# Kernel optimization log

Hardware: AMD Instinct MI355X
Metric: run time of the kernel (lower is better)

## Reference

```python
import jax, jax.numpy as jnp
import numpy as np

B, S, D = 16, 4096, 64
N_HASHES = 8
BUCKET_SIZE = 64
N_BUCKETS = S // BUCKET_SIZE  # 64
NEG = -5e4  # the module uses -50000.0 as masking value
EPS = 1e-6


def setup_inputs() -> dict:
    key = jax.random.key(0)
    k1, k2, k3 = jax.random.split(key, 3)
    qk = jax.random.normal(k1, (B, S, D), dtype=jnp.float32)
    v = jax.random.normal(k2, (B, S, D), dtype=jnp.float32)
    # random rotations for LSH: (batch, dim, n_hashes, n_buckets//2)
    rotations = jax.random.normal(k3, (B, D, N_HASHES, N_BUCKETS // 2), dtype=jnp.float32)
    return {"qk": qk, "v": v, "rotations": rotations, "seed_": 0}


def _look_one_back(x):
    # prepend previous chunk (with wraparound) along the key axis
    x_extra = jnp.concatenate([x[:, -1:], x[:, :-1]], axis=1)
    return jnp.concatenate([x, x_extra], axis=2)


def reference(qk, v, rotations, seed_):
    b, s, d = qk.shape
    n_hashes = rotations.shape[2]
    n_buckets = 2 * rotations.shape[3]
    chunks = n_hashes * n_buckets  # n_bins == n_buckets

    # ---- hash_vectors ----
    rot = jnp.einsum('btf,bfhi->bhti', qk, rotations)          # (b, h, s, nb/2)
    rot = jnp.concatenate([rot, -rot], axis=-1)                # (b, h, s, nb)
    buckets = jnp.argmax(rot, axis=-1)                         # (b, h, s)
    offsets = (jnp.arange(n_hashes) * n_buckets)[None, :, None]
    buckets = (buckets + offsets).reshape(b, n_hashes * s)     # (b, h*s)

    # ---- sort by (bucket, position) ----
    ticker = jnp.arange(n_hashes * s)
    buckets_and_t = s * buckets + (ticker % s)[None, :]
    sticker = jnp.argsort(buckets_and_t, axis=-1)              # stable sort indices
    undo_sort = jnp.argsort(sticker, axis=-1)

    st = sticker % s                                           # original positions
    sqk = jnp.take_along_axis(qk, st[..., None], axis=1)       # (b, h*s, d)
    sv = jnp.take_along_axis(v, st[..., None], axis=1)

    bq_t = st.reshape(b, chunks, -1)                           # (b, chunks, bucket)
    bqk = sqk.reshape(b, chunks, -1, d)
    bv = sv.reshape(b, chunks, -1, d)

    bq = bqk
    norm = jnp.linalg.norm(bqk, axis=-1, keepdims=True)
    bk = bqk / (norm + EPS)                                    # make_unit_length

    bk = _look_one_back(bk)                                    # (b, chunks, 2*bucket, d)
    bv = _look_one_back(bv)
    bkv_t = _look_one_back(bq_t[..., None])[..., 0]            # (b, chunks, 2*bucket)

    dots = jnp.einsum('bhie,bhje->bhij', bq, bk) * (d ** -0.5)
    self_mask = bq_t[:, :, :, None] == bkv_t[:, :, None, :]
    dots = jnp.where(self_mask, NEG, dots)

    dots_lse = jax.nn.logsumexp(dots, axis=-1, keepdims=True)  # (b, chunks, bucket, 1)
    probs = jnp.exp(dots - dots_lse)
    bo = jnp.einsum('buij,buje->buie', probs, bv)              # (b, chunks, bucket, d)

    so = bo.reshape(b, n_hashes * s, d)
    slogits = dots_lse.reshape(b, n_hashes * s)

    # ---- unsort ----
    o = jnp.take_along_axis(so, undo_sort[..., None], axis=1)
    logits = jnp.take_along_axis(slogits, undo_sort, axis=-1)

    # ---- combine hash rounds via logsumexp weights ----
    o = o.reshape(b, n_hashes, s, d)
    logits = logits.reshape(b, n_hashes, s, 1)
    w = jnp.exp(logits - jax.nn.logsumexp(logits, axis=1, keepdims=True))
    out = jnp.sum(o * w, axis=1)                               # (b, s, d)
    return out, buckets
```

## Files before the change

kernel.cpp:

```cpp
#include <hip/hip_runtime.h>
#include <math.h>

#define BB   16
#define SS   4096
#define DD   64
#define HH   8
#define NBH  32
#define NB   64
#define NCH  512

typedef __attribute__((ext_vector_type(8))) short s16x8;
typedef __attribute__((ext_vector_type(4))) short s16x4;
typedef __attribute__((ext_vector_type(4))) float f32x4;
typedef __attribute__((ext_vector_type(4))) unsigned u32x4;

static __device__ __forceinline__ unsigned short f2bf(float x) {
  union { float f; unsigned u; } a; a.f = x;
  unsigned r = a.u + 0x7fffu + ((a.u >> 16) & 1u);
  return (unsigned short)(r >> 16);
}
static __device__ __forceinline__ float bf2f(unsigned short u) {
  union { unsigned u; float f; } a; a.u = ((unsigned)u) << 16;
  return a.f;
}
static __device__ __forceinline__ unsigned bfrnd_hi(float x) {
  union { float f; unsigned u; } a; a.f = x;
  return a.u + 0x7fffu + ((a.u >> 16) & 1u);
}
static __device__ __forceinline__ unsigned pack_bf(float lo, float hi) {
  return __builtin_amdgcn_perm(bfrnd_hi(hi), bfrnd_hi(lo), 0x07060302u);
}

__global__ __launch_bounds__(256) void k_conv(
    const float* __restrict__ qk, const float* __restrict__ v,
    unsigned short* __restrict__ qb, unsigned short* __restrict__ kb,
    unsigned short* __restrict__ vb) {
  const int gid = blockIdx.x * 256 + threadIdx.x;
  const int half = BB * SS * 4;
  const bool isV = gid >= half;
  const int id = isV ? gid - half : gid;
  const int row = id >> 2, q4 = id & 3;

  const float4* src =
      (const float4*)((isV ? v : qk) + (size_t)row * DD + q4 * 16);
  float vals[16];
#pragma unroll
  for (int g = 0; g < 4; g++) {
    const float4 a = src[g];
    vals[g * 4 + 0] = a.x; vals[g * 4 + 1] = a.y;
    vals[g * 4 + 2] = a.z; vals[g * 4 + 3] = a.w;
  }

  if (!isV) {
    float ss = 0.f;
#pragma unroll
    for (int i = 0; i < 16; i++) ss += vals[i] * vals[i];
    ss += __shfl_xor(ss, 1);
    ss += __shfl_xor(ss, 2);
    const float scl = 0.125f / (sqrtf(ss) + 1e-6f);
    unsigned short qo[16], ko[16];
#pragma unroll
    for (int i = 0; i < 16; i++) {
      qo[i] = f2bf(vals[i]);
      ko[i] = f2bf(vals[i] * scl);
    }
    unsigned short* qd = qb + (size_t)row * DD + q4 * 16;
    unsigned short* kd = kb + (size_t)row * DD + q4 * 16;
    *(s16x8*)qd = *(const s16x8*)&qo[0];
    *(s16x8*)(qd + 8) = *(const s16x8*)&qo[8];
    *(s16x8*)kd = *(const s16x8*)&ko[0];
    *(s16x8*)(kd + 8) = *(const s16x8*)&ko[8];
  } else {
    unsigned short vo[16];
#pragma unroll
    for (int i = 0; i < 16; i++) vo[i] = f2bf(vals[i]);
    unsigned short* vd = vb + (size_t)row * DD + q4 * 16;
    *(s16x8*)vd = *(const s16x8*)&vo[0];
    *(s16x8*)(vd + 8) = *(const s16x8*)&vo[8];
  }
}

__global__ __launch_bounds__(256) void k_rotT(
    const float* __restrict__ rot, unsigned short* __restrict__ rTh,
    unsigned short* __restrict__ rTl, int* __restrict__ needy_count) {
  __shared__ float slab[32][256];
  const int b = blockIdx.x;
  const int tid = threadIdx.x;
  if (b == 0 && tid == 0) *needy_count = 0;

  for (int st = 0; st < 2; st++) {
#pragma unroll
    for (int fr = 0; fr < 32; fr++)
      slab[fr][tid] = rot[(size_t)b * (DD * HH * NBH) +
                          (size_t)(st * 32 + fr) * 256 + tid];
    __syncthreads();
    unsigned short hi[32], lo[32];
#pragma unroll
    for (int fr = 0; fr < 32; fr++) {
      const float x = slab[fr][tid];
      const unsigned short hh = f2bf(x);
      hi[fr] = hh;
      lo[fr] = f2bf(x - bf2f(hh));
    }
    unsigned short* dh = rTh + ((size_t)b * 256 + tid) * DD + st * 32;
    unsigned short* dl = rTl + ((size_t)b * 256 + tid) * DD + st * 32;
#pragma unroll
    for (int g = 0; g < 4; g++) {
      *(s16x8*)(dh + g * 8) = *(const s16x8*)&hi[g * 8];
      *(s16x8*)(dl + g * 8) = *(const s16x8*)&lo[g * 8];
    }
    __syncthreads();
  }
}

#define MARGIN 1e-2f

__global__ __launch_bounds__(256, 2) void k_hash_mfma(
    const float* __restrict__ qk, const unsigned short* __restrict__ rTh,
    const unsigned short* __restrict__ rTl, int* __restrict__ bucket_local,
    float* __restrict__ buckets_out, int* __restrict__ needy_list,
    int* __restrict__ needy_count) {
  __shared__ struct __align__(16) {
    unsigned short ah[128][72];
    unsigned short al[128][72];
    float sc[128][33];
  } sm;
  const int b = blockIdx.x;
  const int t0 = blockIdx.y * 128;
  const int tid = threadIdx.x;
  const int w = tid >> 6, lane = tid & 63;
  const int quad = lane >> 4, l16 = lane & 15;

  {
    const int row = tid >> 1, hf = tid & 1;
    const float4* src =
        (const float4*)(qk + ((size_t)b * SS + t0 + row) * DD + hf * 32);
#pragma unroll
    for (int gg = 0; gg < 4; gg++) {
      const float4 v0 = src[gg * 2], v1 = src[gg * 2 + 1];
      const float a[8] = {v0.x, v0.y, v0.z, v0.w, v1.x, v1.y, v1.z, v1.w};
      unsigned short hi[8], lo[8];
#pragma unroll
      for (int e = 0; e < 8; e++) {
        const unsigned short hh = f2bf(a[e]);
        hi[e] = hh;
        lo[e] = f2bf(a[e] - bf2f(hh));
      }
      *(s16x8*)&sm.ah[row][hf * 32 + gg * 8] = *(const s16x8*)hi;
      *(s16x8*)&sm.al[row][hf * 32 + gg * 8] = *(const s16x8*)lo;
    }
  }
  __syncthreads();

  s16x8 Ah[2][2], Al[2][2];
#pragma unroll
  for (int mtl = 0; mtl < 2; mtl++) {
    const int row = (w * 2 + mtl) * 16 + l16;
#pragma unroll
    for (int ks = 0; ks < 2; ks++) {
      Ah[mtl][ks] = *(const s16x8*)&sm.ah[row][ks * 32 + quad * 8];
      Al[mtl][ks] = *(const s16x8*)&sm.al[row][ks * 32 + quad * 8];
    }
  }

#pragma unroll 1
  for (int h = 0; h < HH; h++) {
#pragma unroll
    for (int nt = 0; nt < 2; nt++) {
      const size_t rrow = (((size_t)b * HH + h) * 32 + nt * 16 + l16) * DD;
      s16x8 Bh2[2], Bl2[2];
#pragma unroll
      for (int ks = 0; ks < 2; ks++) {
        Bh2[ks] = *(const s16x8*)&rTh[rrow + ks * 32 + quad * 8];
        Bl2[ks] = *(const s16x8*)&rTl[rrow + ks * 32 + quad * 8];
      }
#pragma unroll
      for (int mtl = 0; mtl < 2; mtl++) {
        f32x4 acc = (f32x4){0.f, 0.f, 0.f, 0.f};
#pragma unroll
        for (int ks = 0; ks < 2; ks++) {
          acc = __builtin_amdgcn_mfma_f32_16x16x32_bf16(Al[mtl][ks], Bl2[ks], acc, 0, 0, 0);
          acc = __builtin_amdgcn_mfma_f32_16x16x32_bf16(Al[mtl][ks], Bh2[ks], acc, 0, 0, 0);
          acc = __builtin_amdgcn_mfma_f32_16x16x32_bf16(Ah[mtl][ks], Bl2[ks], acc, 0, 0, 0);
          acc = __builtin_amdgcn_mfma_f32_16x16x32_bf16(Ah[mtl][ks], Bh2[ks], acc, 0, 0, 0);
        }
#pragma unroll
        for (int r = 0; r < 4; r++)
          sm.sc[(w * 2 + mtl) * 16 + quad * 4 + r][nt * 16 + l16] = acc[r];
      }
    }
    __syncthreads();

    {
      const int l32 = lane & 31;
      const int tloc = w * 32 + l32;
      const bool neg = lane >= 32;
      const float sgn = neg ? -1.0f : 1.0f;
      float best = -3.0e38f, second = -3.0e38f;
      int bi = 0;
#pragma unroll 8
      for (int i = 0; i < 32; i++) {
        const float vv = sgn * sm.sc[tloc][i];
        if (vv > best) { second = best; best = vv; bi = i; }
        else if (vv > second) second = vv;
      }
      if (neg) bi += 32;
      const float ob = __shfl_xor(best, 32);
      const float os = __shfl_xor(second, 32);
      const int obi = __shfl_xor(bi, 32);
      if (lane < 32) {
        const float ms = fmaxf(fminf(best, ob), fmaxf(second, os));
        float mb = best; int mbi = bi;
        if (ob > best) { mb = ob; mbi = obi; }
        const int t = t0 + tloc;
        bucket_local[((size_t)b * HH + h) * SS + t] = mbi;
        buckets_out[(size_t)b * (HH * SS) + (size_t)h * SS + t] =
            (float)(h * NB + mbi);
        if (mb - ms <= MARGIN) {
          const int slot = atomicAdd(needy_count, 1);
          needy_list[slot] = (((b << 3) | h) << 12) | t;
        }
      }
    }
    __syncthreads();
  }
}

__global__ __launch_bounds__(256) void k_hash_fix(
    const float* __restrict__ qk, const float* __restrict__ rot,
    const int* __restrict__ needy_list, const int* __restrict__ needy_count,
    int* __restrict__ bucket_local, float* __restrict__ buckets_out) {
  const int n = *needy_count;
  const int hw = (blockIdx.x * 256 + (int)threadIdx.x) >> 5;
  const int li = threadIdx.x & 31;
  const int nhw = gridDim.x * 8;

  for (int idx = hw; idx < n; idx += nhw) {
    const int code = needy_list[idx];
    const int t = code & 4095;
    const int bh = code >> 12;
    const int b = bh >> 3, h = bh & 7;

    const float* qrow = qk + ((size_t)b * SS + t) * DD;
    const float* rcol = rot + ((size_t)b * DD * HH + h) * NBH + li;

    double acc = 0.0;
#pragma unroll 8
    for (int f = 0; f < DD; f++)
      acc += (double)qrow[f] * (double)rcol[(size_t)f * (HH * NBH)];

    double bv = acc;
    int bi = li;
    if (-acc > bv) { bv = -acc; bi = li + 32; }
#pragma unroll
    for (int off = 1; off < 32; off <<= 1) {
      const double ov = __shfl_xor(bv, off);
      const int oi = __shfl_xor(bi, off);
      if (ov > bv || (ov == bv && oi < bi)) { bv = ov; bi = oi; }
    }
    if (li == 0) {
      bucket_local[((size_t)b * HH + h) * SS + t] = bi;
      buckets_out[(size_t)b * (HH * SS) + (size_t)h * SS + t] =
          (float)(h * NB + bi);
    }
  }
}

__global__ __launch_bounds__(256) void k_sort(
    const int* __restrict__ bucket_local, int* __restrict__ sort_t,
    int* __restrict__ ipos) {
  __shared__ unsigned short lb[SS];
  __shared__ unsigned char  cnt[NB][256];
  __shared__ unsigned short pfx[NB][256];
  __shared__ int part[NB][4];
  __shared__ int tot[NB];
  __shared__ int base[NB];

  const int bh = blockIdx.x;
  const int tid = threadIdx.x;
  const int* src = bucket_local + (size_t)bh * SS;

  int* czero = (int*)&cnt[0][0];
#pragma unroll
  for (int i = 0; i < 16; i++) czero[tid + i * 256] = 0;
  __syncthreads();

#pragma unroll
  for (int i = 0; i < 16; i++) {
    const int t = tid * 16 + i;
    const int v = src[t];
    lb[t] = (unsigned short)v;
    cnt[v][tid]++;
  }
  __syncthreads();

  {
    const int bk = tid & 63, sg = tid >> 6;
    int s = 0;
#pragma unroll 8
    for (int i = 0; i < 64; i++) s += cnt[bk][sg * 64 + i];
    part[bk][sg] = s;
  }
  __syncthreads();
  if (tid < NB) tot[tid] = part[tid][0] + part[tid][1] + part[tid][2] + part[tid][3];
  __syncthreads();
  if (tid == 0) {
    int r = 0;
    for (int i = 0; i < NB; i++) { base[i] = r; r += tot[i]; }
  }
  __syncthreads();
  {
    const int bk = tid & 63, sg = tid >> 6;
    int run = base[bk];
    for (int s = 0; s < sg; s++) run += part[bk][s];
#pragma unroll 8
    for (int i = 0; i < 64; i++) {
      const int th = sg * 64 + i;
      pfx[bk][th] = (unsigned short)run;
      run += cnt[bk][th];
    }
  }
  __syncthreads();
  int* st = sort_t + (size_t)bh * SS;
  int* ip = ipos + (size_t)bh * SS;
#pragma unroll
  for (int i = 0; i < 16; i++) {
    const int t = tid * 16 + i;
    const int bk = lb[t];
    const int pos = pfx[bk][tid]++;
    st[pos] = t;
    ip[t] = pos;
  }
}

__global__ __launch_bounds__(256, 4) void k_attn2(
    const unsigned short* __restrict__ qb, const unsigned short* __restrict__ kbg,
    const unsigned short* __restrict__ vbg, const int* __restrict__ sort_t,
    unsigned short* __restrict__ so, float* __restrict__ lse_u) {
  const int blk = blockIdx.x;
  const int b = blk >> 9;
  const int c = blk & 511;
  const int h = c >> 6, cc = c & 63;
  const int cp = (c + 511) & 511;
  const int hp = cp >> 6, ccp = cp & 63;

  __shared__ struct __align__(16) {
    union {
      unsigned short kb[128][72];
      unsigned short p[64][136];
      float olds[64][68];
    } kp;
    unsigned short vsT[64][136];
    int tk[128];
  } sm;

  const int tid = threadIdx.x;
  const int w = tid >> 6;
  const int lane = tid & 63;
  const int quad = lane >> 4;
  const int l16 = lane & 15;

  if (tid < 128) {
    const size_t srci = (tid < 64)
        ? (((size_t)b * HH + h) * SS + cc * 64 + tid)
        : (((size_t)b * HH + hp) * SS + ccp * 64 + (tid - 64));
    sm.tk[tid] = sort_t[srci];
  }
  __syncthreads();

  {
    const int j = tid >> 1, hf = tid & 1;
    const int trow = sm.tk[j];
    const s16x8* ksrc = (const s16x8*)(kbg + ((size_t)b * SS + trow) * DD + hf * 32);
    s16x8 kr[4];
#pragma unroll
    for (int g = 0; g < 4; g++) kr[g] = ksrc[g];
#pragma unroll
    for (int g = 0; g < 4; g++)
      *(s16x8*)&sm.kp.kb[j][hf * 32 + g * 8] = kr[g];
  }
  {
    const int fg = tid >> 5;
    const int tg = (tid & 31) << 2;
    const unsigned short* vb_b = vbg + (size_t)b * SS * DD + fg * 8;
    const u32x4 a0v = *(const u32x4*)(vb_b + (size_t)sm.tk[tg + 0] * DD);
    const u32x4 a1v = *(const u32x4*)(vb_b + (size_t)sm.tk[tg + 1] * DD);
    const u32x4 a2v = *(const u32x4*)(vb_b + (size_t)sm.tk[tg + 2] * DD);
    const u32x4 a3v = *(const u32x4*)(vb_b + (size_t)sm.tk[tg + 3] * DD);
#pragma unroll
    for (int j = 0; j < 4; j++) {
      uint2 ev, ov;
      ev.x = __builtin_amdgcn_perm(a1v[j], a0v[j], 0x05040100u);
      ev.y = __builtin_amdgcn_perm(a3v[j], a2v[j], 0x05040100u);
      ov.x = __builtin_amdgcn_perm(a1v[j], a0v[j], 0x07060302u);
      ov.y = __builtin_amdgcn_perm(a3v[j], a2v[j], 0x07060302u);
      *(uint2*)&sm.vsT[fg * 8 + 2 * j][tg] = ev;
      *(uint2*)&sm.vsT[fg * 8 + 2 * j + 1][tg] = ov;
    }
  }
  const int tq = sm.tk[w * 16 + l16];
  const unsigned short* qrowp = qb + ((size_t)b * SS + tq) * DD;
  const s16x8 a0 = *(const s16x8*)(qrowp + quad * 8);
  const s16x8 a1 = *(const s16x8*)(qrowp + 32 + quad * 8);
  __syncthreads();

  f32x4 acc[8];
#pragma unroll
  for (int nt = 0; nt < 8; nt++) acc[nt] = (f32x4){0.f, 0.f, 0.f, 0.f};
#pragma unroll
  for (int nt = 0; nt < 8; nt++) {
    const s16x8 b0 = *(const s16x8*)&sm.kp.kb[nt * 16 + l16][quad * 8];
    const s16x8 b1 = *(const s16x8*)&sm.kp.kb[nt * 16 + l16][32 + quad * 8];
    acc[nt] = __builtin_amdgcn_mfma_f32_16x16x32_bf16(b0, a0, acc[nt], 0, 0, 0);
    acc[nt] = __builtin_amdgcn_mfma_f32_16x16x32_bf16(b1, a1, acc[nt], 0, 0, 0);
  }

  {
    const bool dm = (quad == (l16 >> 2));
    const int rm = l16 & 3;
#pragma unroll
    for (int nt = 0; nt < 4; nt++)
      if (nt == w) {
#pragma unroll
        for (int r = 0; r < 4; r++)
          if (dm && rm == r) acc[nt][r] = -50000.0f;
      }
  }
  if (cc == 0) {
#pragma unroll
    for (int nt = 4; nt < 8; nt++)
#pragma unroll
      for (int r = 0; r < 4; r++)
        if (sm.tk[nt * 16 + quad * 4 + r] == tq) acc[nt][r] = -50000.0f;
  }

  float mv[8];
#pragma unroll
  for (int nt = 0; nt < 8; nt++)
    mv[nt] = fmaxf(fmaxf(acc[nt][0], acc[nt][1]), fmaxf(acc[nt][2], acc[nt][3]));
  float m = fmaxf(fmaxf(fmaxf(mv[0], mv[1]), fmaxf(mv[2], mv[3])),
                  fmaxf(fmaxf(mv[4], mv[5]), fmaxf(mv[6], mv[7])));
  m = fmaxf(m, __shfl_xor(m, 16));
  m = fmaxf(m, __shfl_xor(m, 32));

  float sv[8];
#pragma unroll
  for (int nt = 0; nt < 8; nt++) {
#pragma unroll
    for (int r = 0; r < 4; r++) acc[nt][r] = __expf(acc[nt][r] - m);
    sv[nt] = (acc[nt][0] + acc[nt][1]) + (acc[nt][2] + acc[nt][3]);
  }
  float s = ((sv[0] + sv[1]) + (sv[2] + sv[3])) +
            ((sv[4] + sv[5]) + (sv[6] + sv[7]));
  s += __shfl_xor(s, 16);
  s += __shfl_xor(s, 32);
  const float inv = 1.0f / s;
  const float lse = __logf(s) + m;

  if (quad == 0)
    lse_u[((size_t)b * SS + tq) * HH + h] = lse;

  __syncthreads();

  {
    const int prow = w * 16 + l16;
#pragma unroll
    for (int nt = 0; nt < 8; nt++) {
      uint2 pv;
      pv.x = pack_bf(acc[nt][0] * inv, acc[nt][1] * inv);
      pv.y = pack_bf(acc[nt][2] * inv, acc[nt][3] * inv);
      *(uint2*)&sm.kp.p[prow][nt * 16 + quad * 4] = pv;
    }
  }
  __syncthreads();

  f32x4 o[4];
#pragma unroll
  for (int nt = 0; nt < 4; nt++) o[nt] = (f32x4){0.f, 0.f, 0.f, 0.f};
  const unsigned short* vrow = &sm.vsT[w * 16 + l16][0];
#pragma unroll
  for (int kc = 0; kc < 4; kc++) {
    const s16x8 av = *(const s16x8*)(vrow + kc * 32 + quad * 8);
#pragma unroll
    for (int nt = 0; nt < 4; nt++) {
      const s16x8 bp = *(const s16x8*)&sm.kp.p[nt * 16 + l16][kc * 32 + quad * 8];
      o[nt] = __builtin_amdgcn_mfma_f32_16x16x32_bf16(av, bp, o[nt], 0, 0, 0);
    }
  }

  __syncthreads();

#pragma unroll
  for (int nt = 0; nt < 4; nt++)
    *(f32x4*)&sm.kp.olds[nt * 16 + l16][w * 16 + quad * 4] = o[nt];
  __syncthreads();

  {
    const int q = tid >> 2, qt = tid & 3;
    const int t = sm.tk[q];
    float vals[16];
    *(f32x4*)&vals[0]  = *(const f32x4*)&sm.kp.olds[q][qt * 16 + 0];
    *(f32x4*)&vals[4]  = *(const f32x4*)&sm.kp.olds[q][qt * 16 + 4];
    *(f32x4*)&vals[8]  = *(const f32x4*)&sm.kp.olds[q][qt * 16 + 8];
    *(f32x4*)&vals[12] = *(const f32x4*)&sm.kp.olds[q][qt * 16 + 12];
    unsigned pk[8];
#pragma unroll
    for (int g = 0; g < 8; g++) pk[g] = pack_bf(vals[2 * g], vals[2 * g + 1]);
    unsigned short* dst =
        so + (((size_t)b * SS + t) * HH + h) * DD + qt * 16;
    *(uint4*)dst = *(const uint4*)&pk[0];
    *(uint4*)(dst + 8) = *(const uint4*)&pk[4];
  }
}

__global__ __launch_bounds__(256) void k_combine2(
    const unsigned short* __restrict__ so, const float* __restrict__ lse_u,
    float* __restrict__ out) {
  const size_t idx = (size_t)blockIdx.x * 256 + threadIdx.x;
  const int f = (int)(idx & 63);
  const size_t bt = idx >> 6;

  float l[HH];
#pragma unroll
  for (int h = 0; h < HH; h++) l[h] = lse_u[bt * HH + h];
  float m = l[0];
#pragma unroll
  for (int h = 1; h < HH; h++) m = fmaxf(m, l[h]);
  float den = 0.f, num = 0.f;
#pragma unroll
  for (int h = 0; h < HH; h++) {
    const float wgt = __expf(l[h] - m);
    den += wgt;
    num += wgt * bf2f(so[(bt * HH + h) * DD + f]);
  }
  out[idx] = num / den;
}

__global__ __launch_bounds__(256, 2) void k_hash_f32(
    const float* __restrict__ qk, const float* __restrict__ rot,
    int* __restrict__ bucket_local, float* __restrict__ buckets_out,
    int* __restrict__ needy_list, int* __restrict__ needy_count) {
  __shared__ float lb[128 * 65];
  const int b = blockIdx.x;
  const int t0 = blockIdx.y * 128;
  const int tid = threadIdx.x;

  {
    const int row = tid >> 1, hf = (tid & 1) * 32;
    const float4* src =
        (const float4*)(qk + ((size_t)b * SS + t0 + row) * DD + hf);
    float* dst = &lb[row * 65 + hf];
#pragma unroll
    for (int g = 0; g < 8; g++) {
      const float4 vv = src[g];
      dst[g * 4 + 0] = vv.x; dst[g * 4 + 1] = vv.y;
      dst[g * 4 + 2] = vv.z; dst[g * 4 + 3] = vv.w;
    }
  }
  __syncthreads();

  const int w = tid >> 6;
  const int l = tid & 63;
  const int hb = __builtin_amdgcn_readfirstlane(w);

  for (int hp = 0; hp < 2; hp++) {
    const int h = hb + hp * 4;
    const float* rbase = rot + ((size_t)b * DD * HH + h) * NBH;
    const size_t rstride = HH * NBH;

    float acc0[NBH], acc1[NBH];
#pragma unroll
    for (int i = 0; i < NBH; i++) { acc0[i] = 0.f; acc1[i] = 0.f; }

    float4 bufA[8], bufB[8];
#pragma unroll
    for (int i4 = 0; i4 < 8; i4++) bufA[i4] = ((const float4*)rbase)[i4];

    for (int f = 0; f < DD; f += 2) {
      {
        const float4* r4 = (const float4*)(rbase + (size_t)(f + 1) * rstride);
#pragma unroll
        for (int i4 = 0; i4 < 8; i4++) bufB[i4] = r4[i4];
      }
      {
        const float q0 = lb[l * 65 + f];
        const float q1 = lb[(l + 64) * 65 + f];
#pragma unroll
        for (int i4 = 0; i4 < 8; i4++) {
          const float4 rv = bufA[i4];
          acc0[i4*4+0] = fmaf(q0, rv.x, acc0[i4*4+0]);
          acc0[i4*4+1] = fmaf(q0, rv.y, acc0[i4*4+1]);
          acc0[i4*4+2] = fmaf(q0, rv.z, acc0[i4*4+2]);
          acc0[i4*4+3] = fmaf(q0, rv.w, acc0[i4*4+3]);
          acc1[i4*4+0] = fmaf(q1, rv.x, acc1[i4*4+0]);
          acc1[i4*4+1] = fmaf(q1, rv.y, acc1[i4*4+1]);
          acc1[i4*4+2] = fmaf(q1, rv.z, acc1[i4*4+2]);
          acc1[i4*4+3] = fmaf(q1, rv.w, acc1[i4*4+3]);
        }
      }
      if (f + 2 < DD) {
        const float4* r4 = (const float4*)(rbase + (size_t)(f + 2) * rstride);
#pragma unroll
        for (int i4 = 0; i4 < 8; i4++) bufA[i4] = r4[i4];
      }
      {
        const float q0 = lb[l * 65 + f + 1];
        const float q1 = lb[(l + 64) * 65 + f + 1];
#pragma unroll
        for (int i4 = 0; i4 < 8; i4++) {
          const float4 rv = bufB[i4];
          acc0[i4*4+0] = fmaf(q0, rv.x, acc0[i4*4+0]);
          acc0[i4*4+1] = fmaf(q0, rv.y, acc0[i4*4+1]);
          acc0[i4*4+2] = fmaf(q0, rv.z, acc0[i4*4+2]);
          acc0[i4*4+3] = fmaf(q0, rv.w, acc0[i4*4+3]);
          acc1[i4*4+0] = fmaf(q1, rv.x, acc1[i4*4+0]);
          acc1[i4*4+1] = fmaf(q1, rv.y, acc1[i4*4+1]);
          acc1[i4*4+2] = fmaf(q1, rv.z, acc1[i4*4+2]);
          acc1[i4*4+3] = fmaf(q1, rv.w, acc1[i4*4+3]);
        }
      }
    }

#pragma unroll
    for (int tok = 0; tok < 2; tok++) {
      const float* acc = tok ? acc1 : acc0;
      float best = -3.0e38f, second = -3.0e38f;
      int bi = 0;
#pragma unroll
      for (int i = 0; i < 64; i++) {
        const float vv = (i < NBH) ? acc[i] : -acc[i - NBH];
        if (vv > best) { second = best; best = vv; bi = i; }
        else if (vv > second) { second = vv; }
      }
      const int t = t0 + tok * 64 + l;
      bucket_local[((size_t)b * HH + h) * SS + t] = bi;
      buckets_out[(size_t)b * (HH * SS) + (size_t)h * SS + t] =
          (float)(h * NB + bi);
      if (best - second <= MARGIN) {
        const int slot = atomicAdd(needy_count, 1);
        needy_list[slot] = (((b << 3) | h) << 12) | t;
      }
    }
  }
}

__global__ __launch_bounds__(256) void k_attn_atomic(
    const float* __restrict__ qk, const float* __restrict__ v,
    const int* __restrict__ sort_t, float* __restrict__ num,
    float* __restrict__ den) {
  const int blk = blockIdx.x;
  const int b = blk >> 9;
  const int c = blk & 511;
  const int h = c >> 6, cc = c & 63;
  const int cp = (c + 511) & 511;
  const int hp = cp >> 6, ccp = cp & 63;

  __shared__ union {
    struct {
      float qt[DD * 64];
      float kt[DD * 128];
      int   tq[64];
      int   tk[128];
      float nrm[128];
      float red[16 * 64];
      float rmax[64];
      float rsum[64];
    } a;
    struct {
      float pt[128 * 64];
      float vs[128 * 64];
    } p;
  } sm;

  const int tid = threadIdx.x;

  if (tid < 64)
    sm.a.tq[tid] = sort_t[((size_t)b * HH + h) * SS + cc * 64 + tid];
  if (tid >= 128) {
    const int j = tid - 128;
    const size_t src = (j < 64) ? (((size_t)b * HH + h) * SS + cc * 64 + j)
                                : (((size_t)b * HH + hp) * SS + ccp * 64 + (j - 64));
    sm.a.tk[j] = sort_t[src];
  }
  if (tid >= 64 && tid < 192) sm.a.nrm[tid - 64] = 0.f;
  __syncthreads();

  {
    const int qi = tid >> 2, qq = tid & 3;
    const float4* qsrc =
        (const float4*)(qk + ((size_t)b * SS + sm.a.tq[qi]) * DD) + qq * 4;
#pragma unroll
    for (int k4 = 0; k4 < 4; k4++) {
      float4 val = qsrc[k4];
      const int f = qq * 16 + k4 * 4;
      sm.a.qt[(f + 0) * 64 + qi] = val.x;
      sm.a.qt[(f + 1) * 64 + qi] = val.y;
      sm.a.qt[(f + 2) * 64 + qi] = val.z;
      sm.a.qt[(f + 3) * 64 + qi] = val.w;
    }
    const int j = tid >> 1, hhf = tid & 1;
    const float4* ksrc =
        (const float4*)(qk + ((size_t)b * SS + sm.a.tk[j]) * DD) + hhf * 8;
    float ss = 0.f;
#pragma unroll
    for (int k4 = 0; k4 < 8; k4++) {
      float4 val = ksrc[k4];
      const int f = hhf * 32 + k4 * 4;
      sm.a.kt[(f + 0) * 128 + j] = val.x;
      sm.a.kt[(f + 1) * 128 + j] = val.y;
      sm.a.kt[(f + 2) * 128 + j] = val.z;
      sm.a.kt[(f + 3) * 128 + j] = val.w;
      ss += val.x * val.x + val.y * val.y + val.z * val.z + val.w * val.w;
    }
    atomicAdd(&sm.a.nrm[j], ss);
  }
  __syncthreads();
  if (tid < 128) {
    const float n = sqrtf(sm.a.nrm[tid]) + 1e-6f;
    sm.a.nrm[tid] = 0.125f / n;
  }
  float4 vreg[8];
  {
    const int j = tid >> 1, hhf = tid & 1;
    const float4* vsrc =
        (const float4*)(v + ((size_t)b * SS + sm.a.tk[j]) * DD) + hhf * 8;
#pragma unroll
    for (int k4 = 0; k4 < 8; k4++) vreg[k4] = vsrc[k4];
  }
  __syncthreads();

  const int qi0 = (tid & 15) * 4;
  const int j0g = (tid >> 4) * 8;
  const int kg = tid >> 4;
  float acc[4][8];
#pragma unroll
  for (int i = 0; i < 4; i++)
#pragma unroll
    for (int j = 0; j < 8; j++) acc[i][j] = 0.f;

#pragma unroll 8
  for (int f = 0; f < DD; f++) {
    float4 qv = *(const float4*)&sm.a.qt[f * 64 + qi0];
    float4 k0 = *(const float4*)&sm.a.kt[f * 128 + j0g];
    float4 k1 = *(const float4*)&sm.a.kt[f * 128 + j0g + 4];
    float qa[4] = {qv.x, qv.y, qv.z, qv.w};
    float ka[8] = {k0.x, k0.y, k0.z, k0.w, k1.x, k1.y, k1.z, k1.w};
#pragma unroll
    for (int i = 0; i < 4; i++)
#pragma unroll
      for (int j = 0; j < 8; j++) acc[i][j] = fmaf(qa[i], ka[j], acc[i][j]);
  }

  int tqr[4];
#pragma unroll
  for (int i = 0; i < 4; i++) tqr[i] = sm.a.tq[qi0 + i];
  int tkr[8]; float scl[8];
#pragma unroll
  for (int j = 0; j < 8; j++) {
    tkr[j] = sm.a.tk[j0g + j];
    scl[j] = sm.a.nrm[j0g + j];
  }
#pragma unroll
  for (int i = 0; i < 4; i++)
#pragma unroll
    for (int j = 0; j < 8; j++) {
      const float dv = acc[i][j] * scl[j];
      acc[i][j] = (tqr[i] == tkr[j]) ? -50000.0f : dv;
    }

  float pmax[4];
#pragma unroll
  for (int i = 0; i < 4; i++) {
    float m = acc[i][0];
#pragma unroll
    for (int j = 1; j < 8; j++) m = fmaxf(m, acc[i][j]);
    pmax[i] = m;
  }
#pragma unroll
  for (int i = 0; i < 4; i++) sm.a.red[kg * 64 + qi0 + i] = pmax[i];
  __syncthreads();
  if (tid < 64) {
    float m = -3.0e38f;
#pragma unroll
    for (int g = 0; g < 16; g++) m = fmaxf(m, sm.a.red[g * 64 + tid]);
    sm.a.rmax[tid] = m;
  }
  __syncthreads();
  float psum[4];
#pragma unroll
  for (int i = 0; i < 4; i++) {
    const float rm = sm.a.rmax[qi0 + i];
    float s = 0.f;
#pragma unroll
    for (int j = 0; j < 8; j++) {
      const float e = __expf(acc[i][j] - rm);
      acc[i][j] = e;
      s += e;
    }
    psum[i] = s;
  }
#pragma unroll
  for (int i = 0; i < 4; i++) sm.a.red[kg * 64 + qi0 + i] = psum[i];
  __syncthreads();
  if (tid < 64) {
    float s = 0.f;
#pragma unroll
    for (int g = 0; g < 16; g++) s += sm.a.red[g * 64 + tid];
    sm.a.rsum[tid] = s;
  }
  __syncthreads();
  float lse[4], isum[4];
#pragma unroll
  for (int i = 0; i < 4; i++) {
    const float rm = sm.a.rmax[qi0 + i];
    const float s = sm.a.rsum[qi0 + i];
    isum[i] = 1.0f / s;
    lse[i] = __logf(s) + rm;
  }
  __syncthreads();

#pragma unroll
  for (int j = 0; j < 8; j++)
#pragma unroll
    for (int i = 0; i < 4; i++)
      sm.p.pt[(j0g + j) * 64 + qi0 + i] = acc[i][j] * isum[i];
  {
    const int j = tid >> 1, hhf = tid & 1;
#pragma unroll
    for (int k4 = 0; k4 < 8; k4++)
      *(float4*)&sm.p.vs[j * 64 + hhf * 32 + k4 * 4] = vreg[k4];
  }
  __syncthreads();

  const int f0 = (tid >> 4) * 4;
  float o[4][4];
#pragma unroll
  for (int i = 0; i < 4; i++)
#pragma unroll
    for (int j = 0; j < 4; j++) o[i][j] = 0.f;

#pragma unroll 8
  for (int j = 0; j < 128; j++) {
    float4 pv = *(const float4*)&sm.p.pt[j * 64 + qi0];
    float4 vv = *(const float4*)&sm.p.vs[j * 64 + f0];
    float pa[4] = {pv.x, pv.y, pv.z, pv.w};
    float va[4] = {vv.x, vv.y, vv.z, vv.w};
#pragma unroll
    for (int i = 0; i < 4; i++)
#pragma unroll
      for (int j2 = 0; j2 < 4; j2++) o[i][j2] = fmaf(pa[i], va[j2], o[i][j2]);
  }

#pragma unroll
  for (int i = 0; i < 4; i++) {
    const float w = __expf(lse[i]);
    float* dst = num + ((size_t)b * SS + tqr[i]) * DD + f0;
#pragma unroll
    for (int j = 0; j < 4; j++) atomicAdd(dst + j, o[i][j] * w);
    if (kg == 0) atomicAdd(den + (size_t)b * SS + tqr[i], w);
  }
}

__global__ __launch_bounds__(256) void k_final(float* __restrict__ o,
                                               const float* __restrict__ den) {
  const size_t i = (size_t)blockIdx.x * 256 + threadIdx.x;
  o[i] = o[i] / den[i >> 6];
}

extern "C" void kernel_launch(void* const* d_in, const int* in_sizes, int n_in,
                              void* d_out, int out_size, void* d_ws,
                              size_t ws_size, hipStream_t stream) {
  const float* qk  = (const float*)d_in[0];
  const float* v   = (const float*)d_in[1];
  const float* rot = (const float*)d_in[2];

  float* out_attn = (float*)d_out;
  float* buckets_out = out_attn + (size_t)BB * SS * DD;

  const size_t BHS = (size_t)BB * HH * SS;
  const size_t BSD = (size_t)BB * SS * DD;
  const size_t RT  = (size_t)BB * HH * 32 * DD;
  int* bucket_local = (int*)d_ws;
  int* sort_t = bucket_local + BHS;
  int* ipos = sort_t + BHS;
  float* lse_u = (float*)(ipos + BHS);
  unsigned short* qb16 = (unsigned short*)(lse_u + BHS);
  unsigned short* kb16 = qb16 + BSD;
  unsigned short* vb16 = kb16 + BSD;
  unsigned short* so_u = vb16 + BSD;
  unsigned short* rTh = so_u + BHS * DD;
  unsigned short* rTl = rTh + RT;

  const size_t NEED2 =
      4 * BHS * 4 + 3 * BSD * 2 + BHS * DD * 2 + 2 * RT * 2;

  if (ws_size >= NEED2) {
    k_conv<<<2 * BB * SS * 4 / 256, 256, 0, stream>>>(qk, v, qb16, kb16, vb16);
    k_rotT<<<BB, 256, 0, stream>>>(rot, rTh, rTl, ipos);
    k_hash_mfma<<<dim3(BB, SS / 128), 256, 0, stream>>>(
        qk, rTh, rTl, bucket_local, buckets_out, sort_t, ipos);
    k_hash_fix<<<256, 256, 0, stream>>>(qk, rot, sort_t, ipos, bucket_local,
                                        buckets_out);
    k_sort<<<BB * HH, 256, 0, stream>>>(bucket_local, sort_t, ipos);
    k_attn2<<<BB * NCH, 256, 0, stream>>>(qb16, kb16, vb16, sort_t, so_u, lse_u);
    k_combine2<<<(BB * SS * DD) / 256, 256, 0, stream>>>(so_u, lse_u, out_attn);
  } else {
    float* den = (float*)(sort_t + 2 * BHS);
    hipMemsetAsync(out_attn, 0, (size_t)BB * SS * DD * sizeof(float), stream);
    hipMemsetAsync(den, 0, (size_t)BB * SS * sizeof(float), stream);
    hipMemsetAsync(ipos, 0, sizeof(int), stream);
    k_hash_f32<<<dim3(BB, SS / 128), 256, 0, stream>>>(
        qk, rot, bucket_local, buckets_out, sort_t, ipos);
    k_hash_fix<<<256, 256, 0, stream>>>(qk, rot, sort_t, ipos, bucket_local,
                                        buckets_out);
    k_sort<<<BB * HH, 256, 0, stream>>>(bucket_local, sort_t, ipos);
    k_attn_atomic<<<BB * NCH, 256, 0, stream>>>(qk, v, sort_t, out_attn, den);
    k_final<<<(BB * SS * DD) / 256, 256, 0, stream>>>(out_attn, den);
  }
}
```

Baseline: 210.2 us.

## Halve hash tile, double-buffer score smem, and spread argmax across four lanes

The LSH hash kernel now processes 64 positions per block instead of 128, so the grid doubles and the launch bound rises to allow four blocks per CU. The score buffer is double-buffered by hash parity, which removes the second barrier per hash round. The argmax scan is split across four lanes of 16 columns each and merged with two xor-shuffle steps, with tie-breaking that keeps the lowest index. The intent is more parallelism and shorter serial scans in a small kernel. The hash kernel is a small part of the whole pipeline, so the overall effect is limited.

Result: no change. 209.4 us (-0.4%).

```diff
diff --git a/kernel.cpp b/kernel.cpp
--- a/kernel.cpp
+++ b/kernel.cpp
@@ -115,28 +115,28 @@
 
 #define MARGIN 1e-2f
 
-__global__ __launch_bounds__(256, 2) void k_hash_mfma(
+__global__ __launch_bounds__(256, 4) void k_hash_mfma(
     const float* __restrict__ qk, const unsigned short* __restrict__ rTh,
     const unsigned short* __restrict__ rTl, int* __restrict__ bucket_local,
     float* __restrict__ buckets_out, int* __restrict__ needy_list,
     int* __restrict__ needy_count) {
   __shared__ struct __align__(16) {
-    unsigned short ah[128][72];
-    unsigned short al[128][72];
-    float sc[128][33];
+    unsigned short ah[64][72];
+    unsigned short al[64][72];
+    float sc[2][64][33];
   } sm;
   const int b = blockIdx.x;
-  const int t0 = blockIdx.y * 128;
+  const int t0 = blockIdx.y * 64;
   const int tid = threadIdx.x;
   const int w = tid >> 6, lane = tid & 63;
   const int quad = lane >> 4, l16 = lane & 15;
 
   {
-    const int row = tid >> 1, hf = tid & 1;
+    const int row = tid >> 2, qf = tid & 3;
     const float4* src =
-        (const float4*)(qk + ((size_t)b * SS + t0 + row) * DD + hf * 32);
-#pragma unroll
-    for (int gg = 0; gg < 4; gg++) {
+        (const float4*)(qk + ((size_t)b * SS + t0 + row) * DD + qf * 16);
+#pragma unroll
+    for (int gg = 0; gg < 2; gg++) {
       const float4 v0 = src[gg * 2], v1 = src[gg * 2 + 1];
       const float a[8] = {v0.x, v0.y, v0.z, v0.w, v1.x, v1.y, v1.z, v1.w};
       unsigned short hi[8], lo[8];
@@ -146,25 +146,22 @@
         hi[e] = hh;
         lo[e] = f2bf(a[e] - bf2f(hh));
       }
-      *(s16x8*)&sm.ah[row][hf * 32 + gg * 8] = *(const s16x8*)hi;
-      *(s16x8*)&sm.al[row][hf * 32 + gg * 8] = *(const s16x8*)lo;
-    }
-  }
-  __syncthreads();
-
-  s16x8 Ah[2][2], Al[2][2];
-#pragma unroll
-  for (int mtl = 0; mtl < 2; mtl++) {
-    const int row = (w * 2 + mtl) * 16 + l16;
-#pragma unroll
-    for (int ks = 0; ks < 2; ks++) {
-      Ah[mtl][ks] = *(const s16x8*)&sm.ah[row][ks * 32 + quad * 8];
-      Al[mtl][ks] = *(const s16x8*)&sm.al[row][ks * 32 + quad * 8];
-    }
+      *(s16x8*)&sm.ah[row][qf * 16 + gg * 8] = *(const s16x8*)hi;
+      *(s16x8*)&sm.al[row][qf * 16 + gg * 8] = *(const s16x8*)lo;
+    }
+  }
+  __syncthreads();
+
+  s16x8 Ah[2], Al[2];
+#pragma unroll
+  for (int ks = 0; ks < 2; ks++) {
+    Ah[ks] = *(const s16x8*)&sm.ah[w * 16 + l16][ks * 32 + quad * 8];
+    Al[ks] = *(const s16x8*)&sm.al[w * 16 + l16][ks * 32 + quad * 8];
   }
 
 #pragma unroll 1
   for (int h = 0; h < HH; h++) {
+    const int p = h & 1;
 #pragma unroll
     for (int nt = 0; nt < 2; nt++) {
       const size_t rrow = (((size_t)b * HH + h) * 32 + nt * 16 + l16) * DD;
@@ -174,55 +171,61 @@
         Bh2[ks] = *(const s16x8*)&rTh[rrow + ks * 32 + quad * 8];
         Bl2[ks] = *(const s16x8*)&rTl[rrow + ks * 32 + quad * 8];
       }
-#pragma unroll
-      for (int mtl = 0; mtl < 2; mtl++) {
-        f32x4 acc = (f32x4){0.f, 0.f, 0.f, 0.f};
-#pragma unroll
-        for (int ks = 0; ks < 2; ks++) {
-          acc = __builtin_amdgcn_mfma_f32_16x16x32_bf16(Al[mtl][ks], Bl2[ks], acc, 0, 0, 0);
-          acc = __builtin_amdgcn_mfma_f32_16x16x32_bf16(Al[mtl][ks], Bh2[ks], acc, 0, 0, 0);
-          acc = __builtin_amdgcn_mfma_f32_16x16x32_bf16(Ah[mtl][ks], Bl2[ks], acc, 0, 0, 0);
-          acc = __builtin_amdgcn_mfma_f32_16x16x32_bf16(Ah[mtl][ks], Bh2[ks], acc, 0, 0, 0);
-        }
-#pragma unroll
-        for (int r = 0; r < 4; r++)
-          sm.sc[(w * 2 + mtl) * 16 + quad * 4 + r][nt * 16 + l16] = acc[r];
-      }
+      f32x4 acc = (f32x4){0.f, 0.f, 0.f, 0.f};
+#pragma unroll
+      for (int ks = 0; ks < 2; ks++) {
+        acc = __builtin_amdgcn_mfma_f32_16x16x32_bf16(Al[ks], Bl2[ks], acc, 0, 0, 0);
+        acc = __builtin_amdgcn_mfma_f32_16x16x32_bf16(Al[ks], Bh2[ks], acc, 0, 0, 0);
+        acc = __builtin_amdgcn_mfma_f32_16x16x32_bf16(Ah[ks], Bl2[ks], acc, 0, 0, 0);
+        acc = __builtin_amdgcn_mfma_f32_16x16x32_bf16(Ah[ks], Bh2[ks], acc, 0, 0, 0);
+      }
+#pragma unroll
+      for (int r = 0; r < 4; r++)
+        sm.sc[p][w * 16 + quad * 4 + r][nt * 16 + l16] = acc[r];
     }
     __syncthreads();
 
     {
-      const int l32 = lane & 31;
-      const int tloc = w * 32 + l32;
-      const bool neg = lane >= 32;
-      const float sgn = neg ? -1.0f : 1.0f;
+      const int tloc = w * 16 + l16;
+      const float sgn = (quad >= 2) ? -1.0f : 1.0f;
+      const float* rowp = &sm.sc[p][tloc][(quad & 1) * 16];
       float best = -3.0e38f, second = -3.0e38f;
-      int bi = 0;
+      int bi = quad * 16;
 #pragma unroll 8
-      for (int i = 0; i < 32; i++) {
-        const float vv = sgn * sm.sc[tloc][i];
-        if (vv > best) { second = best; best = vv; bi = i; }
+      for (int i = 0; i < 16; i++) {
+        const float vv = sgn * rowp[i];
+        if (vv > best) { second = best; best = vv; bi = quad * 16 + i; }
         else if (vv > second) second = vv;
       }
-      if (neg) bi += 32;
-      const float ob = __shfl_xor(best, 32);
-      const float os = __shfl_xor(second, 32);
-      const int obi = __shfl_xor(bi, 32);
-      if (lane < 32) {
+      {
+        const float ob = __shfl_xor(best, 16);
+        const float os = __shfl_xor(second, 16);
+        const int obi = __shfl_xor(bi, 16);
         const float ms = fmaxf(fminf(best, ob), fmaxf(second, os));
-        float mb = best; int mbi = bi;
-        if (ob > best) { mb = ob; mbi = obi; }
+        const bool partnerLower = (lane & 16) != 0;
+        if (partnerLower ? (ob >= best) : (ob > best)) { best = ob; bi = obi; }
+        second = ms;
+      }
+      {
+        const float ob = __shfl_xor(best, 32);
+        const float os = __shfl_xor(second, 32);
+        const int obi = __shfl_xor(bi, 32);
+        const float ms = fmaxf(fminf(best, ob), fmaxf(second, os));
+        const bool partnerLower = (lane & 32) != 0;
+        if (partnerLower ? (ob >= best) : (ob > best)) { best = ob; bi = obi; }
+        second = ms;
+      }
+      if (quad == 0) {
         const int t = t0 + tloc;
-        bucket_local[((size_t)b * HH + h) * SS + t] = mbi;
+        bucket_local[((size_t)b * HH + h) * SS + t] = bi;
         buckets_out[(size_t)b * (HH * SS) + (size_t)h * SS + t] =
-            (float)(h * NB + mbi);
-        if (mb - ms <= MARGIN) {
+            (float)(h * NB + bi);
+        if (best - second <= MARGIN) {
           const int slot = atomicAdd(needy_count, 1);
           needy_list[slot] = (((b << 3) | h) << 12) | t;
         }
       }
     }
-    __syncthreads();
   }
 }
 
@@ -897,7 +900,7 @@
   if (ws_size >= NEED2) {
     k_conv<<<2 * BB * SS * 4 / 256, 256, 0, stream>>>(qk, v, qb16, kb16, vb16);
     k_rotT<<<BB, 256, 0, stream>>>(rot, rTh, rTl, ipos);
-    k_hash_mfma<<<dim3(BB, SS / 128), 256, 0, stream>>>(
+    k_hash_mfma<<<dim3(BB, SS / 64), 256, 0, stream>>>(
         qk, rTh, rTl, bucket_local, buckets_out, sort_t, ipos);
     k_hash_fix<<<256, 256, 0, stream>>>(qk, rot, sort_t, ipos, bucket_local,
                                         buckets_out);
```
